# Performance work log

Measured on AMD Instinct MI355X. Metric: run time of the kernel, lower is better.

The kernel has to match this reference:

```python
import jax, jax.numpy as jnp
import numpy as np

N_HEAD = 16
D_HEAD = 64
D_MODEL = 1024
SCALE = 1.0 / D_HEAD ** 0.5


def setup_inputs() -> dict:
    key = jax.random.key(0)
    k1, k2 = jax.random.split(key)
    h = jax.random.normal(k1, (2048, 2, D_MODEL), dtype=jnp.float32)
    # torch Linear weight layout: [out_features, in_features]
    w_qkv = jax.random.normal(k2, (3 * N_HEAD * D_HEAD, D_MODEL), dtype=jnp.float32) * (D_MODEL ** -0.5)
    return {"h": h, "w_qkv": w_qkv}


def reference(h, w_qkv):
    qlen, bsz, _ = h.shape
    heads = h @ w_qkv.T  # [qlen, bsz, 3*n_head*d_head]
    head_q, head_k, head_v = jnp.split(heads, 3, axis=-1)
    head_q = head_q.reshape(qlen, bsz, N_HEAD, D_HEAD)
    head_k = head_k.reshape(qlen, bsz, N_HEAD, D_HEAD)
    head_v = head_v.reshape(qlen, bsz, N_HEAD, D_HEAD)
    attn_score = jnp.einsum('ibnd,jbnd->ijbn', head_q, head_k) * SCALE
    attn_prob = jax.nn.softmax(attn_score, axis=1)  # softmax over key dim j
    # dropout is identity at p=0.0 / eval mode
    attn_vec = jnp.einsum('ijbn,jbnd->ibnd', attn_prob, head_v)
    attn_vec = attn_vec.reshape(qlen, bsz, N_HEAD * D_HEAD)
    return attn_vec, attn_prob
```

## Files before the change

kernel.cpp:

```cpp
#include <hip/hip_runtime.h>

typedef _Float16 f16;
typedef f16 f16x8 __attribute__((ext_vector_type(8)));
typedef f16 f16x4 __attribute__((ext_vector_type(4)));
typedef float f32x4 __attribute__((ext_vector_type(4)));

#define QLEN 2048
#define BSZ 2
#define NH 16
#define DH 64
#define DM 1024
#define NBN (BSZ*NH)
#define SCALE 0.125f

static __device__ __forceinline__ f32x4 mfma16(f16x8 a, f16x8 b, f32x4 c) {
  return __builtin_amdgcn_mfma_f32_16x16x32_f16(a, b, c, 0, 0, 0);
}

static __device__ __forceinline__ void gload_lds16(const void* g, void* l) {
  __builtin_amdgcn_global_load_lds((const __attribute__((address_space(1))) unsigned int*)g,
                                   (__attribute__((address_space(3))) unsigned int*)l,
                                   16, 0, 0);
}

__global__ __launch_bounds__(256) void cvt_f32_f16(const float* __restrict__ s,
                                                   f16* __restrict__ d, int n4) {
  int idx = blockIdx.x * 256 + threadIdx.x;
  if (idx >= n4) return;
  f32x4 v = ((const f32x4*)s)[idx];
  f16x4 o;
#pragma unroll
  for (int q = 0; q < 4; ++q) o[q] = (f16)v[q];
  ((f16x4*)d)[idx] = o;
}

__global__ __launch_bounds__(256) void qkv_gemm(const f16* __restrict__ A, const f16* __restrict__ W,
                                                f16* __restrict__ Qs, f16* __restrict__ Ks,
                                                f16* __restrict__ Vt) {
  __shared__ f16 As[128 * 32];
  __shared__ f16 Bs[128 * 32];
  const int bid = blockIdx.x;
  const int r0 = (bid & 31) << 7;
  const int c0 = (bid >> 5) << 7;
  const int t = threadIdx.x;
  const int lane = t & 63, w = t >> 6;
  const int wr = (w >> 1) << 6, wc = (w & 1) << 6;
  const int l15 = lane & 15, lhi = lane >> 4;

  f32x4 acc[4][4] = {};

  const f16* ga = A + (size_t)(r0 + (t >> 2)) * DM + ((t & 3) << 3);
  const f16* gb = W + (size_t)(c0 + (t >> 2)) * DM + ((t & 3) << 3);
  char* la = (char*)As + w * 1024;
  char* lb = (char*)Bs + w * 1024;

  for (int k0 = 0; k0 < DM; k0 += 32) {
    __syncthreads();
    gload_lds16(ga + k0, la);
    gload_lds16(ga + k0 + (size_t)64 * DM, la + 4096);
    gload_lds16(gb + k0, lb);
    gload_lds16(gb + k0 + (size_t)64 * DM, lb + 4096);
    __syncthreads();
    f16x8 af[4], bf[4];
#pragma unroll
    for (int m = 0; m < 4; ++m)
      af[m] = *(const f16x8*)&As[(wr + m * 16 + l15) * 32 + lhi * 8];
#pragma unroll
    for (int n = 0; n < 4; ++n)
      bf[n] = *(const f16x8*)&Bs[(wc + n * 16 + l15) * 32 + lhi * 8];
#pragma unroll
    for (int m = 0; m < 4; ++m)
#pragma unroll
      for (int n = 0; n < 4; ++n)
        acc[m][n] = mfma16(af[m], bf[n], acc[m][n]);
  }

  const int part = c0 >> 10;
#pragma unroll
  for (int m = 0; m < 4; ++m) {
#pragma unroll
    for (int n = 0; n < 4; ++n) {
#pragma unroll
      for (int q = 0; q < 4; ++q) {
        int r = r0 + wr + m * 16 + lhi * 4 + q;
        int c = c0 + wc + n * 16 + l15;
        int i = r >> 1, b = r & 1;
        int nh = (c >> 6) & 15, d = c & 63;
        int bn = b * 16 + nh;
        f16 v = (f16)acc[m][n][q];
        if (part == 0)       Qs[((size_t)bn * QLEN + i) * DH + d] = v;
        else if (part == 1)  Ks[((size_t)bn * QLEN + i) * DH + d] = v;
        else                 Vt[((size_t)bn * DH + d) * QLEN + i] = v;
      }
    }
  }
}

__global__ __launch_bounds__(256) void flash_attn(const f16* __restrict__ Qs, const f16* __restrict__ Ks,
                                                  const f16* __restrict__ Vt, float* __restrict__ av,
                                                  float* __restrict__ sm, float* __restrict__ srl) {
  __shared__ f16 plds[4][16 * 32];
  const int bid = blockIdx.x;
  const int bn = bid >> 4, ib = bid & 15;
  const int t = threadIdx.x, lane = t & 63, w = t >> 6;
  const int l15 = lane & 15, lhi = lane >> 4;
  const int i0 = (ib << 7) + (w << 5);
  const f16* Qb = Qs + ((size_t)bn << 17);
  const f16* Kb = Ks + ((size_t)bn << 17);
  const f16* Vb = Vt + ((size_t)bn << 17);
  f16* pw = plds[w];

  f16x8 qf[2][2];
#pragma unroll
  for (int rg = 0; rg < 2; ++rg)
#pragma unroll
    for (int kc = 0; kc < 2; ++kc)
      qf[rg][kc] = *(const f16x8*)&Qb[(size_t)(i0 + rg * 16 + l15) * DH + kc * 32 + lhi * 8];

  f32x4 o[2][4] = {};
  float mrun[2][4], lrun[2][4];
#pragma unroll
  for (int rg = 0; rg < 2; ++rg)
#pragma unroll
    for (int q = 0; q < 4; ++q) { mrun[rg][q] = -1e30f; lrun[rg][q] = 0.f; }

  for (int j0 = 0; j0 < QLEN; j0 += 32) {
    f16x8 kf[2][2], vf[4];
#pragma unroll
    for (int jc = 0; jc < 2; ++jc)
#pragma unroll
      for (int kc = 0; kc < 2; ++kc)
        kf[jc][kc] = *(const f16x8*)&Kb[(size_t)(j0 + jc * 16 + l15) * DH + kc * 32 + lhi * 8];
#pragma unroll
    for (int dc = 0; dc < 4; ++dc)
      vf[dc] = *(const f16x8*)&Vb[(size_t)(dc * 16 + l15) * QLEN + j0 + lhi * 8];

#pragma unroll
    for (int rg = 0; rg < 2; ++rg) {
      f32x4 s[2];
#pragma unroll
      for (int jc = 0; jc < 2; ++jc) {
        f32x4 z = {0.f, 0.f, 0.f, 0.f};
        z = mfma16(qf[rg][0], kf[jc][0], z);
        z = mfma16(qf[rg][1], kf[jc][1], z);
        s[jc] = z;
      }
      float p[2][4], alpha[4];
#pragma unroll
      for (int q = 0; q < 4; ++q) {
        float v0 = s[0][q] * SCALE, v1 = s[1][q] * SCALE;
        float tm = fmaxf(v0, v1);
        tm = fmaxf(tm, __shfl_xor(tm, 1));
        tm = fmaxf(tm, __shfl_xor(tm, 2));
        tm = fmaxf(tm, __shfl_xor(tm, 4));
        tm = fmaxf(tm, __shfl_xor(tm, 8));
        float mnew = fmaxf(mrun[rg][q], tm);
        alpha[q] = __expf(mrun[rg][q] - mnew);
        mrun[rg][q] = mnew;
        p[0][q] = __expf(v0 - mnew);
        p[1][q] = __expf(v1 - mnew);
        float r = p[0][q] + p[1][q];
        r += __shfl_xor(r, 1);
        r += __shfl_xor(r, 2);
        r += __shfl_xor(r, 4);
        r += __shfl_xor(r, 8);
        lrun[rg][q] = lrun[rg][q] * alpha[q] + r;
      }
#pragma unroll
      for (int dc = 0; dc < 4; ++dc)
#pragma unroll
        for (int q = 0; q < 4; ++q)
          o[rg][dc][q] *= alpha[q];
#pragma unroll
      for (int jc = 0; jc < 2; ++jc)
#pragma unroll
        for (int q = 0; q < 4; ++q)
          pw[(lhi * 4 + q) * 32 + jc * 16 + l15] = (f16)p[jc][q];
      f16x8 pa = *(const f16x8*)&pw[l15 * 32 + lhi * 8];
#pragma unroll
      for (int dc = 0; dc < 4; ++dc)
        o[rg][dc] = mfma16(pa, vf[dc], o[rg][dc]);
    }
  }

  const int b = bn >> 4, nh = bn & 15;
#pragma unroll
  for (int rg = 0; rg < 2; ++rg)
#pragma unroll
    for (int dc = 0; dc < 4; ++dc)
#pragma unroll
      for (int q = 0; q < 4; ++q) {
        int i = i0 + rg * 16 + lhi * 4 + q;
        av[((size_t)i * BSZ + b) * (NH * DH) + nh * DH + dc * 16 + l15] =
            o[rg][dc][q] / lrun[rg][q];
      }
  if (l15 == 0) {
#pragma unroll
    for (int rg = 0; rg < 2; ++rg)
#pragma unroll
      for (int q = 0; q < 4; ++q) {
        int i = i0 + rg * 16 + lhi * 4 + q;
        sm[bn * QLEN + i] = mrun[rg][q];
        srl[bn * QLEN + i] = 1.0f / lrun[rg][q];
      }
  }
}

__global__ __launch_bounds__(256) void write_probs(const f16* __restrict__ Qs, const f16* __restrict__ Ks,
                                                   const float* __restrict__ sm, const float* __restrict__ srl,
                                                   float* __restrict__ pout) {
  __shared__ float tile[16 * 32 * 32];
  const int bid = blockIdx.x;
  const int it = bid >> 6, jt = bid & 63;
  const int i0 = it << 4, j0 = jt << 5;
  const int t = threadIdx.x, lane = t & 63, w = t >> 6;
  const int l15 = lane & 15, lhi = lane >> 4;

#pragma unroll
  for (int bl = 0; bl < 8; ++bl) {
    const int bn = w * 8 + bl;
    const f16* Qb = Qs + ((size_t)bn << 17);
    const f16* Kb = Ks + ((size_t)bn << 17);
    f16x8 qf[2], kf[2][2];
#pragma unroll
    for (int kc = 0; kc < 2; ++kc)
      qf[kc] = *(const f16x8*)&Qb[(size_t)(i0 + l15) * DH + kc * 32 + lhi * 8];
#pragma unroll
    for (int jc = 0; jc < 2; ++jc)
#pragma unroll
      for (int kc = 0; kc < 2; ++kc)
        kf[jc][kc] = *(const f16x8*)&Kb[(size_t)(j0 + jc * 16 + l15) * DH + kc * 32 + lhi * 8];
    f32x4 s[2];
#pragma unroll
    for (int jc = 0; jc < 2; ++jc) {
      f32x4 z = {0.f, 0.f, 0.f, 0.f};
      z = mfma16(qf[0], kf[jc][0], z);
      z = mfma16(qf[1], kf[jc][1], z);
      s[jc] = z;
    }
    float mm[4], rl[4];
#pragma unroll
    for (int q = 0; q < 4; ++q) {
      int i = i0 + lhi * 4 + q;
      mm[q] = sm[bn * QLEN + i];
      rl[q] = srl[bn * QLEN + i];
    }
#pragma unroll
    for (int jc = 0; jc < 2; ++jc)
#pragma unroll
      for (int q = 0; q < 4; ++q) {
        float v = __expf(s[jc][q] * SCALE - mm[q]) * rl[q];
        int i_l = lhi * 4 + q;
        int j_l = jc * 16 + l15;
        int g = ((bn >> 2) ^ (j_l & 7));
        tile[(i_l * 32 + j_l) * 32 + (g << 2) + (bn & 3)] = v;
      }
  }
  __syncthreads();

  const int j_r = t >> 3;
  const int bq = t & 7;
  const int gsw = bq ^ (j_r & 7);
  float* orow = pout + ((size_t)i0 * QLEN + j0 + j_r) * NBN + bq * 4;
#pragma unroll
  for (int r = 0; r < 16; ++r) {
    f32x4 v = *(const f32x4*)&tile[(r * 32 + j_r) * 32 + (gsw << 2)];
    __builtin_nontemporal_store(v, (f32x4*)(orow + (size_t)r * QLEN * NBN));
  }
}

extern "C" void kernel_launch(void* const* d_in, const int* in_sizes, int n_in,
                              void* d_out, int out_size, void* d_ws, size_t ws_size,
                              hipStream_t stream) {
  const float* h  = (const float*)d_in[0];
  const float* wq = (const float*)d_in[1];
  float* av   = (float*)d_out;
  float* pout = av + (size_t)QLEN * BSZ * NH * DH;

  char* ws = (char*)d_ws;
  f16* hh  = (f16*)ws;
  f16* wh  = (f16*)(ws + (8u << 20));
  f16* Qsc = (f16*)(ws + (16u << 20));
  f16* Ksc = (f16*)(ws + (24u << 20));
  f16* Vtc = (f16*)(ws + (32u << 20));
  float* smv  = (float*)(ws + (40u << 20));
  float* srlv = (float*)(ws + (40u << 20) + (QLEN * NBN * 4));

  const int nh4 = QLEN * BSZ * DM / 4;
  const int nw4 = 3 * NH * DH * DM / 4;
  cvt_f32_f16<<<nh4 / 256, 256, 0, stream>>>(h, hh, nh4);
  cvt_f32_f16<<<nw4 / 256, 256, 0, stream>>>(wq, wh, nw4);
  qkv_gemm<<<32 * 24, 256, 0, stream>>>(hh, wh, Qsc, Ksc, Vtc);
  flash_attn<<<NBN * 16, 256, 0, stream>>>(Qsc, Ksc, Vtc, av, smv, srlv);
  write_probs<<<128 * 64, 256, 0, stream>>>(Qsc, Ksc, smv, srlv, pout);
}
```

Before: 389.8 us.

## Restructure probability writer into persistent double-buffered chunk loop with f16 staging

New measurement: 373.4 us. 4.2% less time.

```diff
diff --git a/kernel.cpp b/kernel.cpp
--- a/kernel.cpp
+++ b/kernel.cpp
@@ -21,6 +21,13 @@
   __builtin_amdgcn_global_load_lds((const __attribute__((address_space(1))) unsigned int*)g,
                                    (__attribute__((address_space(3))) unsigned int*)l,
                                    16, 0, 0);
+}
+
+static __device__ __forceinline__ void barrier_lds() {
+  __builtin_amdgcn_sched_barrier(0);
+  asm volatile("s_waitcnt lgkmcnt(0)" ::: "memory");
+  __builtin_amdgcn_s_barrier();
+  __builtin_amdgcn_sched_barrier(0);
 }
 
 __global__ __launch_bounds__(256) void cvt_f32_f16(const float* __restrict__ s,
@@ -206,66 +213,92 @@
   }
 }
 
-__global__ __launch_bounds__(256) void write_probs(const f16* __restrict__ Qs, const f16* __restrict__ Ks,
-                                                   const float* __restrict__ sm, const float* __restrict__ srl,
-                                                   float* __restrict__ pout) {
-  __shared__ float tile[16 * 32 * 32];
+#define LOADK(buf, chn)                                                        \
+  do {                                                                         \
+    _Pragma("unroll") for (int bl_ = 0; bl_ < 4; ++bl_) {                      \
+      const f16* Kb_ = Ks + (((size_t)(w4 + bl_)) << 17) +                     \
+                       (size_t)(j0 + (chn) * 16 + l15) * DH + lhi * 8;         \
+      buf[bl_][0] = *(const f16x8*)(Kb_);                                      \
+      buf[bl_][1] = *(const f16x8*)(Kb_ + 32);                                 \
+    }                                                                          \
+  } while (0)
+
+#define CHUNK(cur, nxt, ch)                                                    \
+  do {                                                                         \
+    const int jbase_ = j0 + (ch) * 16;                                         \
+    f16 stv[4][4];                                                             \
+    _Pragma("unroll") for (int bl_ = 0; bl_ < 4; ++bl_) {                      \
+      f32x4 z = {0.f, 0.f, 0.f, 0.f};                                          \
+      z = mfma16(qf[bl_][0], cur[bl_][0], z);                                  \
+      z = mfma16(qf[bl_][1], cur[bl_][1], z);                                  \
+      _Pragma("unroll") for (int q_ = 0; q_ < 4; ++q_)                         \
+        stv[bl_][q_] = (f16)(__expf(z[q_] * SCALE - mm[bl_][q_]) * rl[bl_][q_]); \
+    }                                                                          \
+    __builtin_amdgcn_sched_barrier(0);                                         \
+    { const int nch_ = ((ch) + 1 < 16) ? (ch) + 1 : 15; LOADK(nxt, nch_); }    \
+    __builtin_amdgcn_sched_barrier(0);                                         \
+    f16* tb_ = tile[(ch) & 1];                                                 \
+    _Pragma("unroll") for (int q_ = 0; q_ < 4; ++q_) {                         \
+      const int i_l = lhi * 4 + q_;                                            \
+      const int jl = l15;                                                      \
+      f16x4 v = {stv[0][q_], stv[1][q_], stv[2][q_], stv[3][q_]};              \
+      *(f16x4*)&tb_[(i_l * 16 + jl) * 32 + ((w ^ (jl & 7)) << 2)] = v;         \
+    }                                                                          \
+    barrier_lds();                                                             \
+    _Pragma("unroll") for (int p_ = 0; p_ < 2; ++p_) {                         \
+      const int i_l = p_ * 8 + w;                                              \
+      f16x8 v = *(const f16x8*)&tb_[(i_l * 16 + jl_s) * 32 + (quad << 3)];     \
+      f16x4 vl = {v[0], v[1], v[2], v[3]};                                     \
+      f16x4 vh = {v[4], v[5], v[6], v[7]};                                     \
+      f16x4 fa = hsw ? vh : vl;                                                \
+      f16x4 fb = hsw ? vl : vh;                                                \
+      f32x4 lo = {(float)fa[0], (float)fa[1], (float)fa[2], (float)fa[3]};     \
+      f32x4 hi = {(float)fb[0], (float)fb[1], (float)fb[2], (float)fb[3]};     \
+      float* op = pout + ((size_t)(i0 + i_l) * QLEN + jbase_ + jl_s) * NBN + o * 8; \
+      *(f32x4*)op = lo;                                                        \
+      *(f32x4*)(op + 4) = hi;                                                  \
+    }                                                                          \
+  } while (0)
+
+__global__ __launch_bounds__(512, 1) void write_probs(const f16* __restrict__ Qs, const f16* __restrict__ Ks,
+                                                      const float* __restrict__ sm, const float* __restrict__ srl,
+                                                      float* __restrict__ pout) {
+  __shared__ f16 tile[2][16 * 16 * 32];
   const int bid = blockIdx.x;
-  const int it = bid >> 6, jt = bid & 63;
-  const int i0 = it << 4, j0 = jt << 5;
+  const int it = bid >> 3, jt = bid & 7;
+  const int i0 = it << 4, j0 = jt << 8;
   const int t = threadIdx.x, lane = t & 63, w = t >> 6;
   const int l15 = lane & 15, lhi = lane >> 4;
-
-#pragma unroll
-  for (int bl = 0; bl < 8; ++bl) {
-    const int bn = w * 8 + bl;
+  const int w4 = w * 4;
+
+  f16x8 qf[4][2];
+  float mm[4][4], rl[4][4];
+#pragma unroll
+  for (int bl = 0; bl < 4; ++bl) {
+    const int bn = w4 + bl;
     const f16* Qb = Qs + ((size_t)bn << 17);
-    const f16* Kb = Ks + ((size_t)bn << 17);
-    f16x8 qf[2], kf[2][2];
 #pragma unroll
     for (int kc = 0; kc < 2; ++kc)
-      qf[kc] = *(const f16x8*)&Qb[(size_t)(i0 + l15) * DH + kc * 32 + lhi * 8];
-#pragma unroll
-    for (int jc = 0; jc < 2; ++jc)
-#pragma unroll
-      for (int kc = 0; kc < 2; ++kc)
-        kf[jc][kc] = *(const f16x8*)&Kb[(size_t)(j0 + jc * 16 + l15) * DH + kc * 32 + lhi * 8];
-    f32x4 s[2];
-#pragma unroll
-    for (int jc = 0; jc < 2; ++jc) {
-      f32x4 z = {0.f, 0.f, 0.f, 0.f};
-      z = mfma16(qf[0], kf[jc][0], z);
-      z = mfma16(qf[1], kf[jc][1], z);
-      s[jc] = z;
+      qf[bl][kc] = *(const f16x8*)&Qb[(size_t)(i0 + l15) * DH + kc * 32 + lhi * 8];
+#pragma unroll
+    for (int q = 0; q < 4; ++q) {
+      const int i = i0 + lhi * 4 + q;
+      mm[bl][q] = sm[bn * QLEN + i];
+      rl[bl][q] = srl[bn * QLEN + i];
     }
-    float mm[4], rl[4];
-#pragma unroll
-    for (int q = 0; q < 4; ++q) {
-      int i = i0 + lhi * 4 + q;
-      mm[q] = sm[bn * QLEN + i];
-      rl[q] = srl[bn * QLEN + i];
-    }
-#pragma unroll
-    for (int jc = 0; jc < 2; ++jc)
-#pragma unroll
-      for (int q = 0; q < 4; ++q) {
-        float v = __expf(s[jc][q] * SCALE - mm[q]) * rl[q];
-        int i_l = lhi * 4 + q;
-        int j_l = jc * 16 + l15;
-        int g = ((bn >> 2) ^ (j_l & 7));
-        tile[(i_l * 32 + j_l) * 32 + (g << 2) + (bn & 3)] = v;
-      }
-  }
-  __syncthreads();
-
-  const int j_r = t >> 3;
-  const int bq = t & 7;
-  const int gsw = bq ^ (j_r & 7);
-  float* orow = pout + ((size_t)i0 * QLEN + j0 + j_r) * NBN + bq * 4;
-#pragma unroll
-  for (int r = 0; r < 16; ++r) {
-    f32x4 v = *(const f32x4*)&tile[(r * 32 + j_r) * 32 + (gsw << 2)];
-    __builtin_nontemporal_store(v, (f32x4*)(orow + (size_t)r * QLEN * NBN));
+  }
+
+  const int o = t & 3;
+  const int jl_s = (t >> 2) & 15;
+  const int quad = o ^ ((jl_s & 7) >> 1);
+  const bool hsw = (jl_s & 1);
+
+  f16x8 kfA[4][2], kfB[4][2];
+  LOADK(kfA, 0);
+
+  for (int ch = 0; ch < 16; ch += 2) {
+    CHUNK(kfA, kfB, ch);
+    CHUNK(kfB, kfA, ch + 1);
   }
 }
 
@@ -292,5 +325,5 @@
   cvt_f32_f16<<<nw4 / 256, 256, 0, stream>>>(wq, wh, nw4);
   qkv_gemm<<<32 * 24, 256, 0, stream>>>(hh, wh, Qsc, Ksc, Vtc);
   flash_attn<<<NBN * 16, 256, 0, stream>>>(Qsc, Ksc, Vtc, av, smv, srlv);
-  write_probs<<<128 * 64, 256, 0, stream>>>(Qsc, Ksc, smv, srlv, pout);
-}
+  write_probs<<<128 * 8, 512, 0, stream>>>(Qsc, Ksc, smv, srlv, pout);
+}
```
